# Kernel optimization log

Measured on AMD Instinct MI355X. Metric: run time of the kernel, lower is better.

Reference implementation:

```python
import jax, jax.numpy as jnp
import numpy as np

B, S, D = 4, 2048, 1024  # batch, seq_len, input_dim == output_dim (dk)


def setup_inputs() -> dict:
    key = jax.random.key(0)
    kx, kq, kk, kv = jax.random.split(key, 4)
    # xavier_uniform bound for square [D, D] matrices
    bound = float(np.sqrt(6.0 / (D + D)))
    return {
        "x": jax.random.normal(kx, (B, S, D), dtype=jnp.float32),
        "WQ": jax.random.uniform(kq, (D, D), jnp.float32, -bound, bound),
        "WK": jax.random.uniform(kk, (D, D), jnp.float32, -bound, bound),
        "WV": jax.random.uniform(kv, (D, D), jnp.float32, -bound, bound),
    }


def reference(x, WQ, WK, WV):
    dk = WQ.shape[1]
    q = x @ WQ  # [B, S, dk]
    k = x @ WK
    v = x @ WV
    scores = jnp.einsum("bsd,btd->bst", q, k) / jnp.sqrt(jnp.asarray(dk, x.dtype))
    # causal mask: tril ones -> positions where mask==0 set to -inf
    s = x.shape[1]
    causal = jnp.tril(jnp.ones((s, s), dtype=bool))
    scores = jnp.where(causal[None, :, :], scores, jnp.asarray(-jnp.inf, x.dtype))
    attention = jax.nn.softmax(scores, axis=-1)
    # NOTE: original applies attention_dropout to `scores` post-softmax and
    # discards the result -> dead op; eval-mode output is attention @ v.
    return jnp.einsum("bst,btd->bsd", attention, v)
```

## Files before the change

### kernel.cpp

```cpp
#include <hip/hip_runtime.h>
#include <stdint.h>


typedef unsigned short u16;
typedef __attribute__((ext_vector_type(8))) short shortx8;
typedef __attribute__((ext_vector_type(4))) float floatx4;

static constexpr int BB = 4;
static constexpr int SS = 2048;
static constexpr int DD = 1024;

__device__ __forceinline__ u16 f2bf(float f) {
  union { float f; uint32_t u; } c; c.f = f;
  uint32_t u = c.u;
  return (u16)((u + 0x7fffu + ((u >> 16) & 1u)) >> 16);
}

#define GLOAD_LDS16(g, l)                                                              \
  __builtin_amdgcn_global_load_lds((const __attribute__((address_space(1))) void*)(g), \
                                   (__attribute__((address_space(3))) void*)(l), 16, 0, 0)

__device__ __forceinline__ void gemm_core_128(
    const u16* __restrict__ A, const u16* __restrict__ Bt,
    int lda, int ldb, int m0, int n0, int kend, floatx4 acc[4][4])
{
  __shared__ u16 lA[128 * 32];
  __shared__ u16 lB[128 * 32];
  const int t = threadIdx.x;
  const int w = t >> 6, l = t & 63;
  const int wm = w >> 1, wn = w & 1;
  const int sr = l >> 2;
  const int sc = (l & 3) * 8;

#pragma unroll
  for (int i = 0; i < 4; ++i)
#pragma unroll
    for (int j = 0; j < 4; ++j)
      acc[i][j] = (floatx4){0.f, 0.f, 0.f, 0.f};

  const u16* Ab = A + (size_t)m0 * lda;
  const u16* Bb = Bt + (size_t)n0 * ldb;

  for (int k0 = 0; k0 < kend; k0 += 32) {
#pragma unroll
    for (int i = 0; i < 2; ++i) {
      const int row = w * 32 + i * 16;
      GLOAD_LDS16(Ab + (size_t)(row + sr) * lda + k0 + sc, &lA[row * 32]);
      GLOAD_LDS16(Bb + (size_t)(row + sr) * ldb + k0 + sc, &lB[row * 32]);
    }
    __syncthreads();

    shortx8 af[4], bf[4];
#pragma unroll
    for (int i = 0; i < 4; ++i)
      af[i] = *(const shortx8*)&lA[(wm * 64 + i * 16 + (l & 15)) * 32 + (l >> 4) * 8];
#pragma unroll
    for (int i = 0; i < 4; ++i)
      bf[i] = *(const shortx8*)&lB[(wn * 64 + i * 16 + (l & 15)) * 32 + (l >> 4) * 8];
#pragma unroll
    for (int i = 0; i < 4; ++i)
#pragma unroll
      for (int j = 0; j < 4; ++j)
        acc[i][j] = __builtin_amdgcn_mfma_f32_16x16x32_bf16(af[i], bf[j], acc[i][j], 0, 0, 0);
    __syncthreads();
  }
}

__global__ __launch_bounds__(256) void x_convert(const float* __restrict__ x,
                                                 u16* __restrict__ xb) {
  const size_t i = (size_t)blockIdx.x * 256 + threadIdx.x;
  float4 v = ((const float4*)x)[i];
  ushort4 o;
  o.x = f2bf(v.x); o.y = f2bf(v.y); o.z = f2bf(v.z); o.w = f2bf(v.w);
  ((ushort4*)xb)[i] = o;
}

__global__ __launch_bounds__(256) void wt_build(const float* __restrict__ WQ,
                                                const float* __restrict__ WK,
                                                const float* __restrict__ WV,
                                                u16* __restrict__ Wt) {
  __shared__ float tile[64][65];
  const int wsel = blockIdx.z;
  const float* W = wsel == 0 ? WQ : (wsel == 1 ? WK : WV);
  const int k0 = blockIdx.y * 64, n0 = blockIdx.x * 64;
  const int tx = threadIdx.x, ty = threadIdx.y;
#pragma unroll
  for (int i = 0; i < 16; ++i)
    tile[ty + i * 4][tx] = W[(size_t)(k0 + ty + i * 4) * DD + n0 + tx];
  __syncthreads();
  u16* dst = Wt + (size_t)wsel * DD * DD;
#pragma unroll
  for (int i = 0; i < 16; ++i)
    dst[(size_t)(n0 + ty + i * 4) * DD + k0 + tx] = f2bf(tile[tx][ty + i * 4]);
}

__global__ __launch_bounds__(256, 2) void qkv_gemm(const u16* __restrict__ x,
                                                   const u16* __restrict__ Wt,
                                                   u16* __restrict__ Q,
                                                   u16* __restrict__ K,
                                                   u16* __restrict__ V) {
  const int m0 = blockIdx.x * 128;
  const int n0t = blockIdx.y * 128;
  floatx4 acc[4][4];
  gemm_core_128(x, Wt, DD, DD, m0, n0t, DD, acc);

  u16* out;
  int n0;
  if (n0t < 1024)      { out = Q; n0 = n0t; }
  else if (n0t < 2048) { out = K; n0 = n0t - 1024; }
  else                 { out = V; n0 = n0t - 2048; }

  const int t = threadIdx.x, w = t >> 6, l = t & 63;
  const int wm = w >> 1, wn = w & 1;
#pragma unroll
  for (int i = 0; i < 4; ++i)
#pragma unroll
    for (int j = 0; j < 4; ++j)
#pragma unroll
      for (int r = 0; r < 4; ++r) {
        const int m = m0 + wm * 64 + i * 16 + (l >> 4) * 4 + r;
        const int n = n0 + wn * 64 + j * 16 + (l & 15);
        out[(size_t)m * DD + n] = f2bf(acc[i][j][r]);
      }
}

__global__ __launch_bounds__(256) void v_transpose(const u16* __restrict__ V,
                                                   u16* __restrict__ Vt) {
  __shared__ u16 tile[64][65];
  const int b = blockIdx.z;
  const int r0 = blockIdx.y * 64, c0 = blockIdx.x * 64;
  const u16* src = V + (size_t)b * SS * DD;
  u16* dst = Vt + (size_t)b * DD * SS;
  const int tx = threadIdx.x, ty = threadIdx.y;
#pragma unroll
  for (int i = 0; i < 16; ++i)
    tile[ty + i * 4][tx] = src[(size_t)(r0 + ty + i * 4) * DD + c0 + tx];
  __syncthreads();
#pragma unroll
  for (int i = 0; i < 16; ++i)
    dst[(size_t)(c0 + ty + i * 4) * SS + r0 + tx] = tile[tx][ty + i * 4];
}

__global__ __launch_bounds__(256, 2) void scores_gemm(const u16* __restrict__ Q,
                                                      const u16* __restrict__ Kt,
                                                      float* __restrict__ Sc) {
  const int b = blockIdx.z;
  const int tcode = blockIdx.x;
  int mb = (int)((sqrtf(8.0f * (float)tcode + 1.0f) - 1.0f) * 0.5f);
  while ((mb + 1) * (mb + 2) / 2 <= tcode) ++mb;
  while (mb * (mb + 1) / 2 > tcode) --mb;
  const int nb = tcode - mb * (mb + 1) / 2;
  const int m0 = mb * 128, n0 = nb * 128;

  floatx4 acc[4][4];
  gemm_core_128(Q + (size_t)b * SS * DD, Kt + (size_t)b * SS * DD, DD, DD, m0, n0, DD, acc);

  float* out = Sc + (size_t)b * SS * SS;
  const int t = threadIdx.x, w = t >> 6, l = t & 63;
  const int wm = w >> 1, wn = w & 1;
#pragma unroll
  for (int i = 0; i < 4; ++i)
#pragma unroll
    for (int j = 0; j < 4; ++j)
#pragma unroll
      for (int r = 0; r < 4; ++r) {
        const int m = m0 + wm * 64 + i * 16 + (l >> 4) * 4 + r;
        const int n = n0 + wn * 64 + j * 16 + (l & 15);
        out[(size_t)m * SS + n] = acc[i][j][r] * 0.03125f;
      }
}

__global__ __launch_bounds__(256) void softmax_causal(const float* __restrict__ Sc,
                                                      u16* __restrict__ P) {
  const int row = blockIdx.x * 4 + (threadIdx.x >> 6);
  const int l = threadIdx.x & 63;
  const int b = row >> 11, i = row & 2047;
  const float* s = Sc + (size_t)b * SS * SS + (size_t)i * SS;
  u16* p = P + (size_t)b * SS * SS + (size_t)i * SS;
  const int n = i + 1;
  const int jend = (i + 128) & ~127;
  const int nc = (jend + 255) >> 8;

  float4 v[8];
  float mx = -INFINITY;
#pragma unroll
  for (int c = 0; c < 8; ++c) {
    if (c < nc) {
      const int col = (c * 64 + l) * 4;
      float4 a = *(const float4*)(s + col);
      a.x = (col + 0 < n) ? a.x : -INFINITY;
      a.y = (col + 1 < n) ? a.y : -INFINITY;
      a.z = (col + 2 < n) ? a.z : -INFINITY;
      a.w = (col + 3 < n) ? a.w : -INFINITY;
      v[c] = a;
      mx = fmaxf(mx, fmaxf(fmaxf(a.x, a.y), fmaxf(a.z, a.w)));
    }
  }
#pragma unroll
  for (int o = 32; o > 0; o >>= 1) mx = fmaxf(mx, __shfl_xor(mx, o, 64));

  float sum = 0.f;
#pragma unroll
  for (int c = 0; c < 8; ++c) {
    if (c < nc) {
      float4 a = v[c];
      a.x = __expf(a.x - mx);
      a.y = __expf(a.y - mx);
      a.z = __expf(a.z - mx);
      a.w = __expf(a.w - mx);
      v[c] = a;
      sum += (a.x + a.y) + (a.z + a.w);
    }
  }
#pragma unroll
  for (int o = 32; o > 0; o >>= 1) sum += __shfl_xor(sum, o, 64);
  const float inv = 1.0f / sum;

#pragma unroll
  for (int c = 0; c < 8; ++c) {
    if (c < nc) {
      const int col = (c * 64 + l) * 4;
      ushort4 o4;
      o4.x = f2bf(v[c].x * inv);
      o4.y = f2bf(v[c].y * inv);
      o4.z = f2bf(v[c].z * inv);
      o4.w = f2bf(v[c].w * inv);
      *(ushort4*)(p + col) = o4;
    }
  }
}

__global__ __launch_bounds__(256, 2) void pv_gemm(const u16* __restrict__ P,
                                                  const u16* __restrict__ Vt,
                                                  float* __restrict__ out) {
  const int b = blockIdx.z;
  const int mb = 15 - blockIdx.y;
  const int m0 = mb * 128, n0 = blockIdx.x * 128;
  floatx4 acc[4][4];
  gemm_core_128(P + (size_t)b * SS * SS, Vt + (size_t)b * DD * SS, SS, SS, m0, n0, m0 + 128, acc);

  float* o = out + (size_t)b * SS * DD;
  const int t = threadIdx.x, w = t >> 6, l = t & 63;
  const int wm = w >> 1, wn = w & 1;
#pragma unroll
  for (int i = 0; i < 4; ++i)
#pragma unroll
    for (int j = 0; j < 4; ++j)
#pragma unroll
      for (int r = 0; r < 4; ++r) {
        const int m = m0 + wm * 64 + i * 16 + (l >> 4) * 4 + r;
        const int n = n0 + wn * 64 + j * 16 + (l & 15);
        o[(size_t)m * DD + n] = acc[i][j][r];
      }
}

extern "C" void kernel_launch(void* const* d_in, const int* in_sizes, int n_in,
                              void* d_out, int out_size, void* d_ws, size_t ws_size,
                              hipStream_t stream) {
  const float* x  = (const float*)d_in[0];
  const float* WQ = (const float*)d_in[1];
  const float* WK = (const float*)d_in[2];
  const float* WV = (const float*)d_in[3];
  float* out = (float*)d_out;

  char* ws = (char*)d_ws;
  const size_t WT_OFF = 0;
  const size_t XB_OFF = WT_OFF + (size_t)3072 * 1024 * 2;
  const size_t Q_OFF  = XB_OFF + (size_t)BB * SS * DD * 2;
  const size_t K_OFF  = Q_OFF + (size_t)BB * SS * DD * 2;
  const size_t V_OFF  = K_OFF + (size_t)BB * SS * DD * 2;
  const size_t VT_OFF = V_OFF + (size_t)BB * SS * DD * 2;
  const size_t P_OFF  = VT_OFF + (size_t)BB * SS * DD * 2;
  const size_t SC_OFF = P_OFF + (size_t)BB * SS * SS * 2;
  u16*   Wt = (u16*)(ws + WT_OFF);
  u16*   xb = (u16*)(ws + XB_OFF);
  u16*   Q  = (u16*)(ws + Q_OFF);
  u16*   Kb = (u16*)(ws + K_OFF);
  u16*   V  = (u16*)(ws + V_OFF);
  u16*   Vt = (u16*)(ws + VT_OFF);
  u16*   P  = (u16*)(ws + P_OFF);
  float* Sc = (float*)(ws + SC_OFF);

  hipLaunchKernelGGL(x_convert, dim3(8192), dim3(256), 0, stream, x, xb);
  hipLaunchKernelGGL(wt_build, dim3(16, 16, 3), dim3(64, 4), 0, stream, WQ, WK, WV, Wt);
  hipLaunchKernelGGL(qkv_gemm, dim3(64, 24), dim3(256), 0, stream, xb, Wt, Q, Kb, V);
  hipLaunchKernelGGL(v_transpose, dim3(16, 32, 4), dim3(64, 4), 0, stream, V, Vt);
  hipLaunchKernelGGL(scores_gemm, dim3(136, 1, 4), dim3(256), 0, stream, Q, Kb, Sc);
  hipLaunchKernelGGL(softmax_causal, dim3(2048), dim3(256), 0, stream, Sc, P);
  hipLaunchKernelGGL(pv_gemm, dim3(8, 16, 4), dim3(256), 0, stream, P, Vt, out);
}
```

Before: 263.0 us.

## Widen GEMM K-tile, merge prep kernels, write V transposed from QKV GEMM

The shared GEMM core now stages 64-wide K slices instead of 32, running two MFMA sub-steps per load and halving the barrier count per K. The x conversion and weight transpose kernels become one launch, and the QKV GEMM writes V straight into transposed layout with 4-element vector stores, which removes the separate V transpose kernel and the intermediate V buffer. LDS use per block doubles, which may lower occupancy, and the transposed V stores are strided across rows.

```diff
diff --git a/kernel.cpp b/kernel.cpp
--- a/kernel.cpp
+++ b/kernel.cpp
@@ -24,13 +24,13 @@
     const u16* __restrict__ A, const u16* __restrict__ Bt,
     int lda, int ldb, int m0, int n0, int kend, floatx4 acc[4][4])
 {
-  __shared__ u16 lA[128 * 32];
-  __shared__ u16 lB[128 * 32];
+  __shared__ u16 lA[128 * 64];
+  __shared__ u16 lB[128 * 64];
   const int t = threadIdx.x;
   const int w = t >> 6, l = t & 63;
   const int wm = w >> 1, wn = w & 1;
-  const int sr = l >> 2;
-  const int sc = (l & 3) * 8;
+  const int sr = l >> 3;
+  const int sc = (l & 7) * 8;
 
 #pragma unroll
   for (int i = 0; i < 4; ++i)
@@ -41,49 +41,57 @@
   const u16* Ab = A + (size_t)m0 * lda;
   const u16* Bb = Bt + (size_t)n0 * ldb;
 
-  for (int k0 = 0; k0 < kend; k0 += 32) {
-#pragma unroll
-    for (int i = 0; i < 2; ++i) {
-      const int row = w * 32 + i * 16;
-      GLOAD_LDS16(Ab + (size_t)(row + sr) * lda + k0 + sc, &lA[row * 32]);
-      GLOAD_LDS16(Bb + (size_t)(row + sr) * ldb + k0 + sc, &lB[row * 32]);
+  for (int k0 = 0; k0 < kend; k0 += 64) {
+#pragma unroll
+    for (int i = 0; i < 4; ++i) {
+      const int row = w * 32 + i * 8;
+      GLOAD_LDS16(Ab + (size_t)(row + sr) * lda + k0 + sc, &lA[row * 64]);
+      GLOAD_LDS16(Bb + (size_t)(row + sr) * ldb + k0 + sc, &lB[row * 64]);
     }
     __syncthreads();
 
-    shortx8 af[4], bf[4];
-#pragma unroll
-    for (int i = 0; i < 4; ++i)
-      af[i] = *(const shortx8*)&lA[(wm * 64 + i * 16 + (l & 15)) * 32 + (l >> 4) * 8];
-#pragma unroll
-    for (int i = 0; i < 4; ++i)
-      bf[i] = *(const shortx8*)&lB[(wn * 64 + i * 16 + (l & 15)) * 32 + (l >> 4) * 8];
-#pragma unroll
-    for (int i = 0; i < 4; ++i)
-#pragma unroll
-      for (int j = 0; j < 4; ++j)
-        acc[i][j] = __builtin_amdgcn_mfma_f32_16x16x32_bf16(af[i], bf[j], acc[i][j], 0, 0, 0);
+#pragma unroll
+    for (int ks = 0; ks < 2; ++ks) {
+      shortx8 af[4], bf[4];
+#pragma unroll
+      for (int i = 0; i < 4; ++i)
+        af[i] = *(const shortx8*)&lA[(wm * 64 + i * 16 + (l & 15)) * 64 + ks * 32 + (l >> 4) * 8];
+#pragma unroll
+      for (int i = 0; i < 4; ++i)
+        bf[i] = *(const shortx8*)&lB[(wn * 64 + i * 16 + (l & 15)) * 64 + ks * 32 + (l >> 4) * 8];
+#pragma unroll
+      for (int i = 0; i < 4; ++i)
+#pragma unroll
+        for (int j = 0; j < 4; ++j)
+          acc[i][j] = __builtin_amdgcn_mfma_f32_16x16x32_bf16(af[i], bf[j], acc[i][j], 0, 0, 0);
+    }
     __syncthreads();
   }
 }
 
-__global__ __launch_bounds__(256) void x_convert(const float* __restrict__ x,
-                                                 u16* __restrict__ xb) {
-  const size_t i = (size_t)blockIdx.x * 256 + threadIdx.x;
-  float4 v = ((const float4*)x)[i];
-  ushort4 o;
-  o.x = f2bf(v.x); o.y = f2bf(v.y); o.z = f2bf(v.z); o.w = f2bf(v.w);
-  ((ushort4*)xb)[i] = o;
-}
-
-__global__ __launch_bounds__(256) void wt_build(const float* __restrict__ WQ,
-                                                const float* __restrict__ WK,
-                                                const float* __restrict__ WV,
-                                                u16* __restrict__ Wt) {
+__global__ __launch_bounds__(256) void prep(const float* __restrict__ x,
+                                            const float* __restrict__ WQ,
+                                            const float* __restrict__ WK,
+                                            const float* __restrict__ WV,
+                                            u16* __restrict__ xb,
+                                            u16* __restrict__ Wt) {
   __shared__ float tile[64][65];
-  const int wsel = blockIdx.z;
+  const int bid = blockIdx.x;
+  const int t = threadIdx.x;
+  if (bid < 8192) {
+    const size_t i = (size_t)bid * 256 + t;
+    float4 v = ((const float4*)x)[i];
+    ushort4 o;
+    o.x = f2bf(v.x); o.y = f2bf(v.y); o.z = f2bf(v.z); o.w = f2bf(v.w);
+    ((ushort4*)xb)[i] = o;
+    return;
+  }
+  const int r = bid - 8192;
+  const int wsel = r >> 8;
+  const int rr = r & 255;
+  const int k0 = (rr >> 4) * 64, n0 = (rr & 15) * 64;
   const float* W = wsel == 0 ? WQ : (wsel == 1 ? WK : WV);
-  const int k0 = blockIdx.y * 64, n0 = blockIdx.x * 64;
-  const int tx = threadIdx.x, ty = threadIdx.y;
+  const int tx = t & 63, ty = t >> 6;
 #pragma unroll
   for (int i = 0; i < 16; ++i)
     tile[ty + i * 4][tx] = W[(size_t)(k0 + ty + i * 4) * DD + n0 + tx];
@@ -98,20 +106,37 @@
                                                    const u16* __restrict__ Wt,
                                                    u16* __restrict__ Q,
                                                    u16* __restrict__ K,
-                                                   u16* __restrict__ V) {
+                                                   u16* __restrict__ Vt) {
   const int m0 = blockIdx.x * 128;
   const int n0t = blockIdx.y * 128;
   floatx4 acc[4][4];
   gemm_core_128(x, Wt, DD, DD, m0, n0t, DD, acc);
 
-  u16* out;
-  int n0;
-  if (n0t < 1024)      { out = Q; n0 = n0t; }
-  else if (n0t < 2048) { out = K; n0 = n0t - 1024; }
-  else                 { out = V; n0 = n0t - 2048; }
-
   const int t = threadIdx.x, w = t >> 6, l = t & 63;
   const int wm = w >> 1, wn = w & 1;
+
+  if (n0t >= 2048) {
+    const int bb = m0 >> 11;
+    const int s0 = (m0 & 2047) + wm * 64 + (l >> 4) * 4;
+    u16* vt = Vt + (size_t)bb * DD * SS;
+#pragma unroll
+    for (int i = 0; i < 4; ++i)
+#pragma unroll
+      for (int j = 0; j < 4; ++j) {
+        const int n = (n0t - 2048) + wn * 64 + j * 16 + (l & 15);
+        const int s = s0 + i * 16;
+        ushort4 o4;
+        o4.x = f2bf(acc[i][j][0]);
+        o4.y = f2bf(acc[i][j][1]);
+        o4.z = f2bf(acc[i][j][2]);
+        o4.w = f2bf(acc[i][j][3]);
+        *(ushort4*)(vt + (size_t)n * SS + s) = o4;
+      }
+    return;
+  }
+
+  u16* out = (n0t < 1024) ? Q : K;
+  const int n0 = n0t & 1023;
 #pragma unroll
   for (int i = 0; i < 4; ++i)
 #pragma unroll
@@ -122,23 +147,6 @@
         const int n = n0 + wn * 64 + j * 16 + (l & 15);
         out[(size_t)m * DD + n] = f2bf(acc[i][j][r]);
       }
-}
-
-__global__ __launch_bounds__(256) void v_transpose(const u16* __restrict__ V,
-                                                   u16* __restrict__ Vt) {
-  __shared__ u16 tile[64][65];
-  const int b = blockIdx.z;
-  const int r0 = blockIdx.y * 64, c0 = blockIdx.x * 64;
-  const u16* src = V + (size_t)b * SS * DD;
-  u16* dst = Vt + (size_t)b * DD * SS;
-  const int tx = threadIdx.x, ty = threadIdx.y;
-#pragma unroll
-  for (int i = 0; i < 16; ++i)
-    tile[ty + i * 4][tx] = src[(size_t)(r0 + ty + i * 4) * DD + c0 + tx];
-  __syncthreads();
-#pragma unroll
-  for (int i = 0; i < 16; ++i)
-    dst[(size_t)(c0 + ty + i * 4) * SS + r0 + tx] = tile[tx][ty + i * 4];
 }
 
 __global__ __launch_bounds__(256, 2) void scores_gemm(const u16* __restrict__ Q,
@@ -268,23 +276,19 @@
   const size_t XB_OFF = WT_OFF + (size_t)3072 * 1024 * 2;
   const size_t Q_OFF  = XB_OFF + (size_t)BB * SS * DD * 2;
   const size_t K_OFF  = Q_OFF + (size_t)BB * SS * DD * 2;
-  const size_t V_OFF  = K_OFF + (size_t)BB * SS * DD * 2;
-  const size_t VT_OFF = V_OFF + (size_t)BB * SS * DD * 2;
+  const size_t VT_OFF = K_OFF + (size_t)BB * SS * DD * 2;
   const size_t P_OFF  = VT_OFF + (size_t)BB * SS * DD * 2;
   const size_t SC_OFF = P_OFF + (size_t)BB * SS * SS * 2;
   u16*   Wt = (u16*)(ws + WT_OFF);
   u16*   xb = (u16*)(ws + XB_OFF);
   u16*   Q  = (u16*)(ws + Q_OFF);
   u16*   Kb = (u16*)(ws + K_OFF);
-  u16*   V  = (u16*)(ws + V_OFF);
   u16*   Vt = (u16*)(ws + VT_OFF);
   u16*   P  = (u16*)(ws + P_OFF);
   float* Sc = (float*)(ws + SC_OFF);
 
-  hipLaunchKernelGGL(x_convert, dim3(8192), dim3(256), 0, stream, x, xb);
-  hipLaunchKernelGGL(wt_build, dim3(16, 16, 3), dim3(64, 4), 0, stream, WQ, WK, WV, Wt);
-  hipLaunchKernelGGL(qkv_gemm, dim3(64, 24), dim3(256), 0, stream, xb, Wt, Q, Kb, V);
-  hipLaunchKernelGGL(v_transpose, dim3(16, 32, 4), dim3(64, 4), 0, stream, V, Vt);
+  hipLaunchKernelGGL(prep, dim3(8960), dim3(256), 0, stream, x, WQ, WK, WV, xb, Wt);
+  hipLaunchKernelGGL(qkv_gemm, dim3(64, 24), dim3(256), 0, stream, xb, Wt, Q, Kb, Vt);
   hipLaunchKernelGGL(scores_gemm, dim3(136, 1, 4), dim3(256), 0, stream, Q, Kb, Sc);
   hipLaunchKernelGGL(softmax_causal, dim3(2048), dim3(256), 0, stream, Sc, P);
   hipLaunchKernelGGL(pv_gemm, dim3(8, 16, 4), dim3(256), 0, stream, P, Vt, out);
```

After: 262.8 us. No clear change (-0.0%).
